# Performance work log

Measured on AMD Instinct MI355X. Metric: run time of the kernel, lower is better.

## Reference

```python
import jax, jax.numpy as jnp
import numpy as np

# DeepSeek-style MLA decode paged attention (vLLM HPU flat_pa_mla, latent cache path)
B = 32              # batch (decode requests)
H = 16              # q heads (TP shard)
KV_LORA = 512       # kv_lora_rank
ROPE = 64           # qk_rope_head_dim
D = KV_LORA + ROPE  # 576, latent+rope dim
BS = 128            # block_size
BLOCKS_PER_SEQ = 16 # 2048-token context
NB = B * BLOCKS_PER_SEQ   # 512 active blocks
NCACHE = 1024       # blocks in the paged cache
SCALE = 192 ** -0.5  # 1/sqrt(qk_nope(128)+rope(64))
NEG = -1.0e9


def setup_inputs() -> dict:
    key = jax.random.key(0)
    k1, k2, k3, k4 = jax.random.split(key, 4)
    query = jax.random.normal(k1, (B, H, D), dtype=jnp.float32)
    key_cache = jax.random.normal(k2, (NCACHE, BS, D), dtype=jnp.float32)
    # each active block points at some cache block
    block_list = jax.random.randint(k3, (NB,), 0, NCACHE, dtype=jnp.int32)
    # contiguous grouping: blocks_per_seq blocks per request
    block_groups = jnp.repeat(jnp.arange(B, dtype=jnp.int32), BLOCKS_PER_SEQ)
    block_mapping = jax.nn.one_hot(block_groups, B, dtype=jnp.float32)  # [NB, B]
    # per-block usage in [1, BS]; unused tail positions masked out
    usage = jax.random.randint(k4, (NB,), 1, BS + 1)
    block_bias = jnp.where(jnp.arange(BS)[None, :] < usage[:, None], 0.0, NEG).astype(jnp.float32)
    return {"query": query, "key_cache": key_cache, "block_mapping": block_mapping,
            "block_bias": block_bias, "block_list": block_list, "block_groups": block_groups}


def reference(query, key_cache, block_mapping, block_bias, block_list, block_groups):
    # batch2block: scatter per-batch query to its blocks via one-hot matmul
    q = SCALE * jnp.einsum('nb,bhd->nhd', block_mapping, query)      # [NB,H,D]
    kv = key_cache[block_list]                                       # [NB,BS,D] fetched latent KV
    v = kv[..., :KV_LORA]                                            # [NB,BS,V]
    attn = jnp.einsum('nhd,nsd->nhs', q, kv) + block_bias[:, None, :]  # [NB,H,BS]
    # per-block online softmax pieces
    block_max = attn.max(axis=-1, keepdims=True)                     # [NB,H,1]
    p = jnp.exp(attn - block_max)
    block_sums = p.sum(axis=-1)                                      # [NB,H]
    o = jnp.einsum('nhs,nsv->nhv', p, v)                             # [NB,H,V]
    bm = block_max[..., 0]                                           # [NB,H]
    # grouped max over blocks of the same request, broadcast back to blocks
    group_max = jax.ops.segment_max(bm, block_groups, num_segments=B)[block_groups]
    adj = jnp.exp(bm - group_max)                                    # [NB,H]
    sum_adj = block_sums * adj
    # block2batch then batch2block of the adjusted sums
    group_sum = jnp.einsum('nb,nh->bh', block_mapping, sum_adj)
    group_sum = jnp.einsum('nb,bh->nh', block_mapping, group_sum)
    group_sum = jnp.maximum(group_sum, sum_adj)
    rescale = adj / group_sum
    o = o * rescale[..., None]
    # block2batch: sum rescaled partial outputs per request
    out = jnp.einsum('nb,nhv->bhv', block_mapping, o)                # [B,H,V]
    return out
```

## Files before the change

### kernel.cpp

```cpp
#include <hip/hip_runtime.h>
#include <math.h>

#define NB_ 512
#define B_ 32
#define H_ 16
#define D_ 576
#define KV_ 512
#define BS_ 128
#define SCALE_ 0.07216878364870323f

typedef __attribute__((ext_vector_type(8))) short bf16x8;
typedef __attribute__((ext_vector_type(4))) float f32x4;

__device__ float g_o[NB_ * H_ * KV_];
__device__ float g_bm[NB_ * H_];
__device__ float g_bs[NB_ * H_];

static __device__ inline unsigned short f2bf(float f) {
    unsigned int u = __float_as_uint(f);
    unsigned int r = (u + 0x7FFFu + ((u >> 16) & 1u)) >> 16;
    return (unsigned short)r;
}

__global__ __launch_bounds__(256, 3) void mla_block_kernel(
    const float* __restrict__ query,
    const float* __restrict__ key_cache,
    const float* __restrict__ block_bias,
    const int* __restrict__ block_list,
    const int* __restrict__ block_groups)
{
    __shared__ unsigned char region[40960];
    __shared__ float mred[4][16];
    __shared__ float lred[4][16];
    unsigned short* qf = (unsigned short*)region;
    unsigned short* kf = (unsigned short*)(region + 18944);
    float* vt  = (float*)region;
    float* p_s = (float*)(region + 32768);

    const int tid = threadIdx.x;
    const int n   = blockIdx.x;
    const int b   = block_groups[n];
    const float* K = key_cache + (long)block_list[n] * (BS_ * D_);
    const float* Q = query + (long)b * (H_ * D_);

    const int w    = tid >> 6;
    const int lane = tid & 63;
    const int a15  = lane & 15;
    const int q4   = lane >> 4;

#pragma unroll
    for (int i = 0; i < 9; ++i) {
        int flat = tid + 256 * i;
        int row = flat / 144;
        int c4  = flat - row * 144;
        float4 v = *(const float4*)(Q + row * D_ + 4 * c4);
        ushort4 us;
        us.x = f2bf(v.x * SCALE_); us.y = f2bf(v.y * SCALE_);
        us.z = f2bf(v.z * SCALE_); us.w = f2bf(v.w * SCALE_);
        *(ushort4*)(qf + row * 592 + 4 * c4) = us;
    }

    f32x4 acc0 = {0.f, 0.f, 0.f, 0.f};
    f32x4 acc1 = {0.f, 0.f, 0.f, 0.f};
    for (int kk = 0; kk < 9; ++kk) {
        __syncthreads();
#pragma unroll
        for (int i = 0; i < 8; ++i) {
            int flat = tid + 256 * i;
            int s = flat >> 4;
            int bb = flat & 15;
            float4 v = *(const float4*)(K + (long)s * D_ + kk * 64 + 4 * bb);
            ushort4 us;
            us.x = f2bf(v.x); us.y = f2bf(v.y); us.z = f2bf(v.z); us.w = f2bf(v.w);
            *(ushort4*)(kf + s * 72 + 4 * bb) = us;
        }
        __syncthreads();
#pragma unroll
        for (int t = 0; t < 2; ++t) {
            bf16x8 af  = *(bf16x8*)(qf + a15 * 592 + kk * 64 + t * 32 + 8 * q4);
            bf16x8 bf0 = *(bf16x8*)(kf + (32 * w + a15) * 72 + t * 32 + 8 * q4);
            bf16x8 bf1 = *(bf16x8*)(kf + (32 * w + 16 + a15) * 72 + t * 32 + 8 * q4);
            acc0 = __builtin_amdgcn_mfma_f32_16x16x32_bf16(af, bf0, acc0, 0, 0, 0);
            acc1 = __builtin_amdgcn_mfma_f32_16x16x32_bf16(af, bf1, acc1, 0, 0, 0);
        }
    }

    const float* bias = block_bias + n * BS_;
    float b0 = bias[32 * w + a15];
    float b1 = bias[32 * w + 16 + a15];
    float lg0[4], lg1[4], mw[4];
#pragma unroll
    for (int r = 0; r < 4; ++r) {
        lg0[r] = acc0[r] + b0;
        lg1[r] = acc1[r] + b1;
        float m = fmaxf(lg0[r], lg1[r]);
#pragma unroll
        for (int off = 1; off < 16; off <<= 1) m = fmaxf(m, __shfl_xor(m, off));
        mw[r] = m;
    }
    if (a15 == 0) {
#pragma unroll
        for (int r = 0; r < 4; ++r) mred[w][4 * q4 + r] = mw[r];
    }
    __syncthreads();
    float mg[4], lw[4];
#pragma unroll
    for (int r = 0; r < 4; ++r) {
        int h = 4 * q4 + r;
        float m = fmaxf(fmaxf(mred[0][h], mred[1][h]), fmaxf(mred[2][h], mred[3][h]));
        mg[r] = m;
        float p0 = __expf(lg0[r] - m);
        float p1 = __expf(lg1[r] - m);
        p_s[h * BS_ + 32 * w + a15]      = p0;
        p_s[h * BS_ + 32 * w + 16 + a15] = p1;
        float s = p0 + p1;
#pragma unroll
        for (int off = 1; off < 16; off <<= 1) s += __shfl_xor(s, off);
        lw[r] = s;
    }
    if (a15 == 0) {
#pragma unroll
        for (int r = 0; r < 4; ++r) lred[w][4 * q4 + r] = lw[r];
    }
    __syncthreads();
    if (w == 0 && a15 == 0) {
#pragma unroll
        for (int r = 0; r < 4; ++r) {
            int h = 4 * q4 + r;
            g_bm[n * H_ + h] = mg[r];
            g_bs[n * H_ + h] = lred[0][h] + lred[1][h] + lred[2][h] + lred[3][h];
        }
    }

    const int hg = w;
    const int sl = lane;
    float4 oa0[4], oa1[4];
#pragma unroll
    for (int i = 0; i < 4; ++i) {
        oa0[i] = make_float4(0.f, 0.f, 0.f, 0.f);
        oa1[i] = make_float4(0.f, 0.f, 0.f, 0.f);
    }
    for (int sc = 0; sc < 8; ++sc) {
        __syncthreads();
#pragma unroll
        for (int i = 0; i < 8; ++i) {
            int flat = tid + 256 * i;
            int s = flat >> 7;
            int c = (flat & 127) << 2;
            *(float4*)(vt + s * KV_ + c) = *(const float4*)(K + (long)(16 * sc + s) * D_ + c);
        }
        __syncthreads();
#pragma unroll 4
        for (int s = 0; s < 16; ++s) {
            float4 v0 = *(const float4*)(vt + s * KV_ + 4 * sl);
            float4 v1 = *(const float4*)(vt + s * KV_ + 256 + 4 * sl);
#pragma unroll
            for (int i = 0; i < 4; ++i) {
                float pv = p_s[(4 * hg + i) * BS_ + 16 * sc + s];
                oa0[i].x += pv * v0.x; oa0[i].y += pv * v0.y;
                oa0[i].z += pv * v0.z; oa0[i].w += pv * v0.w;
                oa1[i].x += pv * v1.x; oa1[i].y += pv * v1.y;
                oa1[i].z += pv * v1.z; oa1[i].w += pv * v1.w;
            }
        }
    }

    float* op = g_o + (long)n * H_ * KV_;
#pragma unroll
    for (int i = 0; i < 4; ++i) {
        *(float4*)(op + (4 * hg + i) * KV_ + 4 * sl) = oa0[i];
        *(float4*)(op + (4 * hg + i) * KV_ + 256 + 4 * sl) = oa1[i];
    }
}

__global__ __launch_bounds__(128) void mla_combine_kernel(float* __restrict__ out)
{
    const int bh = blockIdx.x;
    const int b = bh >> 4;
    const int h = bh & 15;
    const int tid = threadIdx.x;

    float bm[16];
    float m = -1e30f;
#pragma unroll
    for (int j = 0; j < 16; ++j) {
        bm[j] = g_bm[(16 * b + j) * H_ + h];
        m = fmaxf(m, bm[j]);
    }
    float sa[16];
    float gs = 0.f;
#pragma unroll
    for (int j = 0; j < 16; ++j) {
        sa[j] = g_bs[(16 * b + j) * H_ + h] * __expf(bm[j] - m);
        gs += sa[j];
    }
    float4 acc = make_float4(0.f, 0.f, 0.f, 0.f);
#pragma unroll
    for (int j = 0; j < 16; ++j) {
        float r = __expf(bm[j] - m) / fmaxf(gs, sa[j]);
        const float4 v = *(const float4*)(g_o + ((long)((16 * b + j) * H_ + h)) * KV_ + 4 * tid);
        acc.x += r * v.x; acc.y += r * v.y;
        acc.z += r * v.z; acc.w += r * v.w;
    }
    *(float4*)(out + (long)bh * KV_ + 4 * tid) = acc;
}

extern "C" void kernel_launch(void* const* d_in, const int* in_sizes, int n_in,
                              void* d_out, int out_size, void* d_ws, size_t ws_size,
                              hipStream_t stream)
{
    const float* query        = (const float*)d_in[0];
    const float* key_cache    = (const float*)d_in[1];
    const float* block_bias   = (const float*)d_in[3];
    const int*   block_list   = (const int*)d_in[4];
    const int*   block_groups = (const int*)d_in[5];
    float* out = (float*)d_out;

    mla_block_kernel<<<NB_, 256, 0, stream>>>(query, key_cache, block_bias,
                                              block_list, block_groups);
    mla_combine_kernel<<<B_ * H_, 128, 0, stream>>>(out);
}
```

Baseline: 394.3 us.

## Double-buffer K/V tiles via async global-to-LDS loads and split combine

Replaces the register-staged, bf16-converted K tile loads with asynchronous global_load_lds copies of fp32 data into a swizzled, double-buffered LDS area. The next K chunk, and later V chunks, are fetched while MFMA or FMA work runs on the current one, and the bf16 conversion moves to register time using v_cvt_pk_bf16_f32. Q fragments are held in registers and the scale is applied after the dot product. The combine kernel now uses twice as many blocks, splitting the output columns and the j-range with an LDS reduction. Occupancy drops from 3 to 2 blocks per CU, and the LDS footprint grows to fp32 tiles.

```diff
diff --git a/kernel.cpp b/kernel.cpp
--- a/kernel.cpp
+++ b/kernel.cpp
@@ -16,26 +16,43 @@
 __device__ float g_bm[NB_ * H_];
 __device__ float g_bs[NB_ * H_];
 
-static __device__ inline unsigned short f2bf(float f) {
-    unsigned int u = __float_as_uint(f);
-    unsigned int r = (u + 0x7FFFu + ((u >> 16) & 1u)) >> 16;
-    return (unsigned short)r;
-}
-
-__global__ __launch_bounds__(256, 3) void mla_block_kernel(
+typedef const __attribute__((address_space(1))) void* gp_t;
+typedef __attribute__((address_space(3))) void* lp_t;
+typedef __attribute__((address_space(3))) char* l3p;
+
+static __device__ __forceinline__ void glds16(const float* g, l3p l) {
+    __builtin_amdgcn_global_load_lds((gp_t)g, (lp_t)l, 16, 0, 0);
+}
+
+static __device__ __forceinline__ unsigned int cvtpk(float a, float b) {
+    unsigned int r;
+    asm("v_cvt_pk_bf16_f32 %0, %1, %2" : "=v"(r) : "v"(a), "v"(b));
+    return r;
+}
+
+static __device__ __forceinline__ bf16x8 pack8(float4 a, float4 b) {
+    union { unsigned int u[4]; bf16x8 v; } r;
+    r.u[0] = cvtpk(a.x, a.y);
+    r.u[1] = cvtpk(a.z, a.w);
+    r.u[2] = cvtpk(b.x, b.y);
+    r.u[3] = cvtpk(b.z, b.w);
+    return r.v;
+}
+
+__global__ __launch_bounds__(256, 2) void mla_block_kernel(
     const float* __restrict__ query,
     const float* __restrict__ key_cache,
     const float* __restrict__ block_bias,
     const int* __restrict__ block_list,
     const int* __restrict__ block_groups)
 {
-    __shared__ unsigned char region[40960];
-    __shared__ float mred[4][16];
-    __shared__ float lred[4][16];
-    unsigned short* qf = (unsigned short*)region;
-    unsigned short* kf = (unsigned short*)(region + 18944);
-    float* vt  = (float*)region;
-    float* p_s = (float*)(region + 32768);
+    __shared__ __align__(16) float smem[18560];
+    float* p_s  = smem + 16384;
+    float* mred = smem + 18432;
+    float* lred = smem + 18496;
+
+    const l3p lbase = (l3p)smem;
+    const float* bufp[2] = { smem, smem + 8192 };
 
     const int tid = threadIdx.x;
     const int n   = blockIdx.x;
@@ -47,52 +64,72 @@
     const int lane = tid & 63;
     const int a15  = lane & 15;
     const int q4   = lane >> 4;
-
-#pragma unroll
-    for (int i = 0; i < 9; ++i) {
-        int flat = tid + 256 * i;
-        int row = flat / 144;
-        int c4  = flat - row * 144;
-        float4 v = *(const float4*)(Q + row * D_ + 4 * c4);
-        ushort4 us;
-        us.x = f2bf(v.x * SCALE_); us.y = f2bf(v.y * SCALE_);
-        us.z = f2bf(v.z * SCALE_); us.w = f2bf(v.w * SCALE_);
-        *(ushort4*)(qf + row * 592 + 4 * c4) = us;
-    }
+    const int krow = lane >> 4;
+    const int kgc  = lane & 15;
+
+    const float* bias = block_bias + n * BS_;
+    const float b0 = bias[32 * w + a15];
+    const float b1 = bias[32 * w + 16 + a15];
+
+#pragma unroll
+    for (int j = 0; j < 8; ++j) {
+        int row = w * 32 + j * 4 + krow;
+        glds16(K + row * D_ + 4 * (kgc ^ (row & 7)),
+               lbase + (w * 32 + j * 4) * 256);
+    }
+
+    bf16x8 af[9][2];
+#pragma unroll
+    for (int kk = 0; kk < 9; ++kk)
+#pragma unroll
+        for (int t = 0; t < 2; ++t) {
+            const float* qp = Q + a15 * D_ + kk * 64 + t * 32 + 8 * q4;
+            float4 qa = *(const float4*)qp;
+            float4 qb = *(const float4*)(qp + 4);
+            af[kk][t] = pack8(qa, qb);
+        }
 
     f32x4 acc0 = {0.f, 0.f, 0.f, 0.f};
     f32x4 acc1 = {0.f, 0.f, 0.f, 0.f};
+    const int s0  = 32 * w + a15;
+    const int key = a15 & 7;
+
+#pragma unroll
     for (int kk = 0; kk < 9; ++kk) {
         __syncthreads();
-#pragma unroll
-        for (int i = 0; i < 8; ++i) {
-            int flat = tid + 256 * i;
-            int s = flat >> 4;
-            int bb = flat & 15;
-            float4 v = *(const float4*)(K + (long)s * D_ + kk * 64 + 4 * bb);
-            ushort4 us;
-            us.x = f2bf(v.x); us.y = f2bf(v.y); us.z = f2bf(v.z); us.w = f2bf(v.w);
-            *(ushort4*)(kf + s * 72 + 4 * bb) = us;
-        }
-        __syncthreads();
+        if (kk < 8) {
+#pragma unroll
+            for (int j = 0; j < 8; ++j) {
+                int row = w * 32 + j * 4 + krow;
+                glds16(K + row * D_ + (kk + 1) * 64 + 4 * (kgc ^ (row & 7)),
+                       lbase + ((kk + 1) & 1) * 32768 + (w * 32 + j * 4) * 256);
+            }
+        } else {
+#pragma unroll
+            for (int j = 0; j < 8; ++j) {
+                int fl = (w * 8 + j) * 64 + lane;
+                glds16(K + (fl >> 7) * D_ + 4 * (fl & 127),
+                       lbase + 32768 + (w * 8 + j) * 1024);
+            }
+        }
+        const float* bk = bufp[kk & 1];
 #pragma unroll
         for (int t = 0; t < 2; ++t) {
-            bf16x8 af  = *(bf16x8*)(qf + a15 * 592 + kk * 64 + t * 32 + 8 * q4);
-            bf16x8 bf0 = *(bf16x8*)(kf + (32 * w + a15) * 72 + t * 32 + 8 * q4);
-            bf16x8 bf1 = *(bf16x8*)(kf + (32 * w + 16 + a15) * 72 + t * 32 + 8 * q4);
-            acc0 = __builtin_amdgcn_mfma_f32_16x16x32_bf16(af, bf0, acc0, 0, 0, 0);
-            acc1 = __builtin_amdgcn_mfma_f32_16x16x32_bf16(af, bf1, acc1, 0, 0, 0);
-        }
-    }
-
-    const float* bias = block_bias + n * BS_;
-    float b0 = bias[32 * w + a15];
-    float b1 = bias[32 * w + 16 + a15];
+            int g0 = t * 8 + 2 * q4;
+            float4 a0 = *(const float4*)(bk + s0 * 64        + 4 * ((g0    ) ^ key));
+            float4 a1 = *(const float4*)(bk + s0 * 64        + 4 * ((g0 + 1) ^ key));
+            float4 c0 = *(const float4*)(bk + (s0 + 16) * 64 + 4 * ((g0    ) ^ key));
+            float4 c1 = *(const float4*)(bk + (s0 + 16) * 64 + 4 * ((g0 + 1) ^ key));
+            acc0 = __builtin_amdgcn_mfma_f32_16x16x32_bf16(af[kk][t], pack8(a0, a1), acc0, 0, 0, 0);
+            acc1 = __builtin_amdgcn_mfma_f32_16x16x32_bf16(af[kk][t], pack8(c0, c1), acc1, 0, 0, 0);
+        }
+    }
+
     float lg0[4], lg1[4], mw[4];
 #pragma unroll
     for (int r = 0; r < 4; ++r) {
-        lg0[r] = acc0[r] + b0;
-        lg1[r] = acc1[r] + b1;
+        lg0[r] = SCALE_ * acc0[r] + b0;
+        lg1[r] = SCALE_ * acc1[r] + b1;
         float m = fmaxf(lg0[r], lg1[r]);
 #pragma unroll
         for (int off = 1; off < 16; off <<= 1) m = fmaxf(m, __shfl_xor(m, off));
@@ -100,14 +137,14 @@
     }
     if (a15 == 0) {
 #pragma unroll
-        for (int r = 0; r < 4; ++r) mred[w][4 * q4 + r] = mw[r];
+        for (int r = 0; r < 4; ++r) mred[w * 16 + 4 * q4 + r] = mw[r];
     }
     __syncthreads();
     float mg[4], lw[4];
 #pragma unroll
     for (int r = 0; r < 4; ++r) {
         int h = 4 * q4 + r;
-        float m = fmaxf(fmaxf(mred[0][h], mred[1][h]), fmaxf(mred[2][h], mred[3][h]));
+        float m = fmaxf(fmaxf(mred[h], mred[16 + h]), fmaxf(mred[32 + h], mred[48 + h]));
         mg[r] = m;
         float p0 = __expf(lg0[r] - m);
         float p1 = __expf(lg1[r] - m);
@@ -120,7 +157,7 @@
     }
     if (a15 == 0) {
 #pragma unroll
-        for (int r = 0; r < 4; ++r) lred[w][4 * q4 + r] = lw[r];
+        for (int r = 0; r < 4; ++r) lred[w * 16 + 4 * q4 + r] = lw[r];
     }
     __syncthreads();
     if (w == 0 && a15 == 0) {
@@ -128,7 +165,7 @@
         for (int r = 0; r < 4; ++r) {
             int h = 4 * q4 + r;
             g_bm[n * H_ + h] = mg[r];
-            g_bs[n * H_ + h] = lred[0][h] + lred[1][h] + lred[2][h] + lred[3][h];
+            g_bs[n * H_ + h] = lred[h] + lred[16 + h] + lred[32 + h] + lred[48 + h];
         }
     }
 
@@ -140,27 +177,38 @@
         oa0[i] = make_float4(0.f, 0.f, 0.f, 0.f);
         oa1[i] = make_float4(0.f, 0.f, 0.f, 0.f);
     }
+#pragma unroll
     for (int sc = 0; sc < 8; ++sc) {
         __syncthreads();
-#pragma unroll
-        for (int i = 0; i < 8; ++i) {
-            int flat = tid + 256 * i;
-            int s = flat >> 7;
-            int c = (flat & 127) << 2;
-            *(float4*)(vt + s * KV_ + c) = *(const float4*)(K + (long)(16 * sc + s) * D_ + c);
-        }
-        __syncthreads();
-#pragma unroll 4
-        for (int s = 0; s < 16; ++s) {
-            float4 v0 = *(const float4*)(vt + s * KV_ + 4 * sl);
-            float4 v1 = *(const float4*)(vt + s * KV_ + 256 + 4 * sl);
-#pragma unroll
-            for (int i = 0; i < 4; ++i) {
-                float pv = p_s[(4 * hg + i) * BS_ + 16 * sc + s];
-                oa0[i].x += pv * v0.x; oa0[i].y += pv * v0.y;
-                oa0[i].z += pv * v0.z; oa0[i].w += pv * v0.w;
-                oa1[i].x += pv * v1.x; oa1[i].y += pv * v1.y;
-                oa1[i].z += pv * v1.z; oa1[i].w += pv * v1.w;
+        if (sc < 7) {
+#pragma unroll
+            for (int j = 0; j < 8; ++j) {
+                int fl = (w * 8 + j) * 64 + lane;
+                glds16(K + (long)(16 * (sc + 1) + (fl >> 7)) * D_ + 4 * (fl & 127),
+                       lbase + (sc & 1) * 32768 + (w * 8 + j) * 1024);
+            }
+        }
+        const float* bv = bufp[(sc + 1) & 1];
+#pragma unroll
+        for (int sg = 0; sg < 4; ++sg) {
+            float4 pv[4];
+#pragma unroll
+            for (int i = 0; i < 4; ++i)
+                pv[i] = *(const float4*)(p_s + (4 * hg + i) * BS_ + 16 * sc + 4 * sg);
+#pragma unroll
+            for (int ss = 0; ss < 4; ++ss) {
+                const int s = 4 * sg + ss;
+                float4 v0 = *(const float4*)(bv + s * KV_ + 4 * sl);
+                float4 v1 = *(const float4*)(bv + s * KV_ + 256 + 4 * sl);
+#pragma unroll
+                for (int i = 0; i < 4; ++i) {
+                    const float p = ss == 0 ? pv[i].x : ss == 1 ? pv[i].y
+                                  : ss == 2 ? pv[i].z : pv[i].w;
+                    oa0[i].x += p * v0.x; oa0[i].y += p * v0.y;
+                    oa0[i].z += p * v0.z; oa0[i].w += p * v0.w;
+                    oa1[i].x += p * v1.x; oa1[i].y += p * v1.y;
+                    oa1[i].z += p * v1.z; oa1[i].w += p * v1.w;
+                }
             }
         }
     }
@@ -168,17 +216,21 @@
     float* op = g_o + (long)n * H_ * KV_;
 #pragma unroll
     for (int i = 0; i < 4; ++i) {
-        *(float4*)(op + (4 * hg + i) * KV_ + 4 * sl) = oa0[i];
+        *(float4*)(op + (4 * hg + i) * KV_ + 4 * sl)       = oa0[i];
         *(float4*)(op + (4 * hg + i) * KV_ + 256 + 4 * sl) = oa1[i];
     }
 }
 
 __global__ __launch_bounds__(128) void mla_combine_kernel(float* __restrict__ out)
 {
-    const int bh = blockIdx.x;
+    const int gid  = blockIdx.x;
+    const int bh   = gid >> 1;
+    const int half = gid & 1;
     const int b = bh >> 4;
     const int h = bh & 15;
     const int tid = threadIdx.x;
+    const int c4 = tid & 63;
+    const int jh = tid >> 6;
 
     float bm[16];
     float m = -1e30f;
@@ -194,15 +246,33 @@
         sa[j] = g_bs[(16 * b + j) * H_ + h] * __expf(bm[j] - m);
         gs += sa[j];
     }
+
     float4 acc = make_float4(0.f, 0.f, 0.f, 0.f);
-#pragma unroll
-    for (int j = 0; j < 16; ++j) {
-        float r = __expf(bm[j] - m) / fmaxf(gs, sa[j]);
-        const float4 v = *(const float4*)(g_o + ((long)((16 * b + j) * H_ + h)) * KV_ + 4 * tid);
-        acc.x += r * v.x; acc.y += r * v.y;
-        acc.z += r * v.z; acc.w += r * v.w;
-    }
-    *(float4*)(out + (long)bh * KV_ + 4 * tid) = acc;
+    if (jh == 0) {
+#pragma unroll
+        for (int j = 0; j < 8; ++j) {
+            float r = __expf(bm[j] - m) / fmaxf(gs, sa[j]);
+            const float4 v = *(const float4*)(g_o + ((long)((16 * b + j) * H_ + h)) * KV_
+                                              + half * 256 + 4 * c4);
+            acc.x += r * v.x; acc.y += r * v.y; acc.z += r * v.z; acc.w += r * v.w;
+        }
+    } else {
+#pragma unroll
+        for (int j = 8; j < 16; ++j) {
+            float r = __expf(bm[j] - m) / fmaxf(gs, sa[j]);
+            const float4 v = *(const float4*)(g_o + ((long)((16 * b + j) * H_ + h)) * KV_
+                                              + half * 256 + 4 * c4);
+            acc.x += r * v.x; acc.y += r * v.y; acc.z += r * v.z; acc.w += r * v.w;
+        }
+    }
+    __shared__ float4 red[64];
+    if (jh) red[c4] = acc;
+    __syncthreads();
+    if (!jh) {
+        float4 o2 = red[c4];
+        acc.x += o2.x; acc.y += o2.y; acc.z += o2.z; acc.w += o2.w;
+        *(float4*)(out + (long)bh * KV_ + half * 256 + 4 * c4) = acc;
+    }
 }
 
 extern "C" void kernel_launch(void* const* d_in, const int* in_sizes, int n_in,
@@ -218,5 +288,5 @@
 
     mla_block_kernel<<<NB_, 256, 0, stream>>>(query, key_cache, block_bias,
                                               block_list, block_groups);
-    mla_combine_kernel<<<B_ * H_, 128, 0, stream>>>(out);
-}
+    mla_combine_kernel<<<B_ * H_ * 2, 128, 0, stream>>>(out);
+}
```

After: 462.6 us. 17.3% more time.
